# Kernel tuning notes

Hardware: AMD Instinct MI355X
Metric: run time of the kernel (lower is better)

Reference implementation:

```python
import jax, jax.numpy as jnp
import numpy as np

N_NODES = 50000
N_EDGES = 800000
IN_DIM, HID_DIM, N_CLASS = 128, 128, 2
DROPOUT_P = 0.5
NEG_SLOPE = 0.01  # F.leaky_relu default


def gcn_conv(x, src, dst, W, b, n_nodes):
    """PyG GCNConv: add self-loops, sym-normalize, aggregate, then bias."""
    loops = jnp.arange(n_nodes, dtype=src.dtype)
    s = jnp.concatenate([src, loops])
    d = jnp.concatenate([dst, loops])
    # degree on A + I (edge weights = 1), counted at destination
    deg = jax.ops.segment_sum(jnp.ones_like(d, dtype=x.dtype), d, num_segments=n_nodes)
    dis = jnp.where(deg > 0, jax.lax.rsqrt(deg), 0.0)  # deg^{-1/2}
    norm = dis[s] * dis[d]                               # [E+N]
    h = x @ W                                            # [N, out]
    msg = h[s] * norm[:, None]                           # gather + scale
    out = jax.ops.segment_sum(msg, d, num_segments=n_nodes)  # scatter-add
    return out + b


def dropout(x, p, key):
    keep = 1.0 - p
    mask = jax.random.bernoulli(key, keep, x.shape)
    return jnp.where(mask, x / keep, 0.0)


def setup_inputs() -> dict:
    key = jax.random.key(0)
    ks = jax.random.split(key, 8)
    x = jax.random.normal(ks[0], (N_NODES, IN_DIM), dtype=jnp.float32)
    edge_index = jax.random.randint(ks[1], (2, N_EDGES), 0, N_NODES, dtype=jnp.int64)
    def glorot(k, fin, fout):
        lim = np.sqrt(6.0 / (fin + fout)).astype(np.float32)
        return jax.random.uniform(k, (fin, fout), jnp.float32, -lim, lim)
    W1 = glorot(ks[2], IN_DIM, HID_DIM)
    W2 = glorot(ks[3], HID_DIM, HID_DIM)
    W3 = glorot(ks[4], HID_DIM, N_CLASS)
    b1 = jnp.zeros((HID_DIM,), jnp.float32)
    b2 = jnp.zeros((HID_DIM,), jnp.float32)
    b3 = jnp.zeros((N_CLASS,), jnp.float32)
    return {"x": x, "edge_index": edge_index, "W1": W1, "b1": b1,
            "W2": W2, "b2": b2, "W3": W3, "b3": b3}


def reference(x, edge_index, W1, b1, W2, b2, W3, b3):
    src, dst = edge_index[0], edge_index[1]
    n = x.shape[0]
    dkey = jax.random.key(42)
    k1, k2 = jax.random.split(dkey)
    h = gcn_conv(x, src, dst, W1, b1, n)
    h = jax.nn.leaky_relu(h, NEG_SLOPE)
    h = dropout(h, DROPOUT_P, k1)
    h = gcn_conv(h, src, dst, W2, b2, n)
    h = jax.nn.leaky_relu(h, NEG_SLOPE)
    h = dropout(h, DROPOUT_P, k2)
    h = gcn_conv(h, src, dst, W3, b3, n)
    return jax.nn.log_softmax(h, axis=1)
```

## Files before the change

### kernel.cpp

```cpp
#include <hip/hip_runtime.h>
#include <stdint.h>

#define N_NODES 50000
#define N_EDGES 800000
#define DIM     128
#define NB   196
#define CAP  8192
#define CHUNK 2048
#define NBLK 391
#define GNODES 16
#define GGRID 3125
#define GCAP 2048
#define FN   64
#define FBLK 782
#define GCAP_F 3072
#define G3NODES 128
#define G3CAP 4096
#define ZBLK 98

typedef __attribute__((ext_vector_type(8))) unsigned short ushort8_t;
typedef __attribute__((ext_vector_type(8))) short bfrag;
typedef __attribute__((ext_vector_type(4))) float f32x4;

__host__ __device__ inline void threefry2x32(uint32_t k0, uint32_t k1,
                                             uint32_t x0, uint32_t x1,
                                             uint32_t& o0, uint32_t& o1) {
    uint32_t ks0 = k0, ks1 = k1, ks2 = k0 ^ k1 ^ 0x1BD11BDAu;
    uint32_t v0 = x0 + ks0, v1 = x1 + ks1;
#define TF_R(r) { v0 += v1; v1 = (v1 << (r)) | (v1 >> (32 - (r))); v1 ^= v0; }
    TF_R(13) TF_R(15) TF_R(26) TF_R(6)
    v0 += ks1; v1 += ks2 + 1u;
    TF_R(17) TF_R(29) TF_R(16) TF_R(24)
    v0 += ks2; v1 += ks0 + 2u;
    TF_R(13) TF_R(15) TF_R(26) TF_R(6)
    v0 += ks0; v1 += ks1 + 3u;
    TF_R(17) TF_R(29) TF_R(16) TF_R(24)
    v0 += ks1; v1 += ks2 + 4u;
    TF_R(13) TF_R(15) TF_R(26) TF_R(6)
    v0 += ks2; v1 += ks0 + 5u;
#undef TF_R
    o0 = v0; o1 = v1;
}

__device__ inline float drop_scale(uint32_t kk0, uint32_t kk1, uint32_t i) {
    uint32_t b0, b1;
    threefry2x32(kk0, kk1, 0u, i, b0, b1);
    uint32_t bits = b0 ^ b1;
    return (bits >> 31) ? 0.0f : 2.0f;
}

__device__ inline float bf2f(ushort u) {
    return __uint_as_float(((uint32_t)u) << 16);
}
__device__ inline float bfpair_lo(uint32_t u) { return __uint_as_float(u << 16); }
__device__ inline float bfpair_hi(uint32_t u) { return __uint_as_float(u & 0xffff0000u); }

__device__ inline ushort f2bf_rne(float f) {
    uint32_t bits = __float_as_uint(f);
    uint32_t lsb = (bits >> 16) & 1u;
    bits += 0x7fffu + lsb;
    return (ushort)(bits >> 16);
}

__device__ inline void acc8(float* acc, uint4 u, float d) {
    acc[0] += d * bfpair_lo(u.x); acc[1] += d * bfpair_hi(u.x);
    acc[2] += d * bfpair_lo(u.y); acc[3] += d * bfpair_hi(u.y);
    acc[4] += d * bfpair_lo(u.z); acc[5] += d * bfpair_hi(u.z);
    acc[6] += d * bfpair_lo(u.w); acc[7] += d * bfpair_hi(u.w);
}
__device__ inline void acc8p(float* acc, uint4 u) {
    acc[0] += bfpair_lo(u.x); acc[1] += bfpair_hi(u.x);
    acc[2] += bfpair_lo(u.y); acc[3] += bfpair_hi(u.y);
    acc[4] += bfpair_lo(u.z); acc[5] += bfpair_hi(u.z);
    acc[6] += bfpair_lo(u.w); acc[7] += bfpair_hi(u.w);
}

template<int F32A, int SCALE>
__device__ inline void gemm_body(const ushort* __restrict__ Xb,
                                 const float* __restrict__ Xf,
                                 const ushort* __restrict__ Wt,
                                 const float* __restrict__ dis,
                                 ushort* __restrict__ Hb, int gb, int tid) {
    int w = tid >> 6, lane = tid & 63;
    int m0 = gb * 128 + w * 32;
    int lrow = lane & 15, quad = lane >> 4;
    f32x4 acc[2][8] = {};
    for (int kt = 0; kt < DIM; kt += 32) {
        bfrag a[2], b[8];
        #pragma unroll
        for (int t = 0; t < 2; ++t) {
            int m = m0 + t * 16 + lrow;
            if (m >= N_NODES) m = 0;
            if (F32A) {
                const float* p = Xf + (size_t)m * DIM + kt + quad * 8;
                f32x4 v0 = *(const f32x4*)p;
                f32x4 v1 = *(const f32x4*)(p + 4);
                #pragma unroll
                for (int j = 0; j < 4; ++j) {
                    a[t][j]     = (short)f2bf_rne(v0[j]);
                    a[t][j + 4] = (short)f2bf_rne(v1[j]);
                }
            } else {
                a[t] = *(const bfrag*)(Xb + (size_t)m * DIM + kt + quad * 8);
            }
        }
        #pragma unroll
        for (int c = 0; c < 8; ++c) {
            int n = c * 16 + lrow;
            b[c] = *(const bfrag*)(Wt + (size_t)n * DIM + kt + quad * 8);
        }
        #pragma unroll
        for (int t = 0; t < 2; ++t)
            #pragma unroll
            for (int c = 0; c < 8; ++c)
                acc[t][c] = __builtin_amdgcn_mfma_f32_16x16x32_bf16(a[t], b[c], acc[t][c], 0, 0, 0);
    }
    #pragma unroll
    for (int t = 0; t < 2; ++t) {
        #pragma unroll
        for (int r = 0; r < 4; ++r) {
            int rowi = m0 + t * 16 + quad * 4 + r;
            if (rowi < N_NODES) {
                float dv = SCALE ? dis[rowi] : 1.0f;
                #pragma unroll
                for (int c = 0; c < 8; ++c) {
                    int feat = c * 16 + lrow;
                    float z = SCALE ? acc[t][c][r] * dv : acc[t][c][r];
                    Hb[(size_t)rowi * DIM + feat] = f2bf_rne(z);
                }
            }
        }
    }
}

__global__ __launch_bounds__(256) void k_prep(const float* __restrict__ W1,
                                              const float* __restrict__ W2,
                                              ushort* __restrict__ W1t,
                                              ushort* __restrict__ W2t,
                                              const int* __restrict__ src,
                                              const int* __restrict__ dst,
                                              uint32_t* __restrict__ gcur,
                                              uint32_t* __restrict__ packed,
                                              float* __restrict__ h3s) {
    __shared__ uint32_t h[NB];
    int b = blockIdx.x;
    int t = threadIdx.x;
    if (b < NBLK) {
        uint32_t dc[CHUNK / 256], sc[CHUNK / 256];
        if (t < NB) h[t] = 0u;
        __syncthreads();
        int base = b * CHUNK;
        #pragma unroll
        for (int i = 0; i < CHUNK / 256; ++i) {
            int e = base + i * 256 + t;
            if (e < N_EDGES) {
                dc[i] = (uint32_t)dst[e];
                sc[i] = (uint32_t)src[e];
                atomicAdd(&h[dc[i] >> 8], 1u);
            } else {
                dc[i] = 0xffffffffu;
            }
        }
        __syncthreads();
        if (t < NB) {
            uint32_t c = h[t];
            h[t] = c ? atomicAdd(&gcur[t], c) : 0u;
        }
        __syncthreads();
        #pragma unroll
        for (int i = 0; i < CHUNK / 256; ++i) {
            if (dc[i] != 0xffffffffu) {
                uint32_t d = dc[i];
                uint32_t s = sc[i];
                uint32_t bk = d >> 8;
                uint32_t pos = atomicAdd(&h[bk], 1u);
                if (pos < CAP)
                    packed[(size_t)bk * CAP + pos] = ((d & 255u) << 16) | s;
            }
        }
    } else if (b < NBLK + 128) {
        int j = (b - NBLK) * 256 + t;
        const float* W = (j < DIM * DIM) ? W1 : W2;
        ushort* Wt = (j < DIM * DIM) ? W1t : W2t;
        int i = j & (DIM * DIM - 1);
        int k = i >> 7, n = i & 127;
        Wt[n * DIM + k] = f2bf_rne(W[k * DIM + n]);
    } else {
        int idx = (b - NBLK - 128) * 256 + t;
        if (idx < (N_NODES * 2) / 4) {
            f32x4 z = {0.f, 0.f, 0.f, 0.f};
            ((f32x4*)h3s)[idx] = z;
        }
    }
}

__global__ __launch_bounds__(256) void k_fill(const uint32_t* __restrict__ gcur,
                                              const uint32_t* __restrict__ packed,
                                              uint32_t* __restrict__ row,
                                              float* __restrict__ dis,
                                              ushort* __restrict__ col16,
                                              const float* __restrict__ x,
                                              const ushort* __restrict__ W1t,
                                              ushort* __restrict__ Hb) {
    __shared__ uint32_t sdeg[256];
    __shared__ uint32_t scan[256];
    __shared__ uint32_t cur[256];
    int b = blockIdx.x;
    int t = threadIdx.x;
    if (b >= NB) {
        gemm_body<1, 0>(nullptr, x, W1t, nullptr, Hb, b - NB, t);
        return;
    }
    uint32_t n = gcur[b];
    scan[t] = (t < b) ? gcur[t] : 0u;
    __syncthreads();
    for (int off = 1; off < 256; off <<= 1) {
        uint32_t xx = (t >= off) ? scan[t - off] : 0u;
        __syncthreads();
        scan[t] += xx;
        __syncthreads();
    }
    uint32_t cbase = scan[255];
    __syncthreads();
    uint32_t pbase = (uint32_t)b * CAP;
    sdeg[t] = 0u;
    __syncthreads();
    for (uint32_t i = t; i < n; i += 256) {
        uint32_t u = packed[pbase + i];
        atomicAdd(&sdeg[u >> 16], 1u);
    }
    __syncthreads();
    uint32_t myd = sdeg[t];
    scan[t] = myd;
    __syncthreads();
    for (int off = 1; off < 256; off <<= 1) {
        uint32_t xx = (t >= off) ? scan[t - off] : 0u;
        __syncthreads();
        scan[t] += xx;
        __syncthreads();
    }
    uint32_t excl = scan[t] - myd;
    cur[t] = excl;
    int v = b * 256 + t;
    if (v <= N_NODES) row[v] = cbase + excl;
    if (v < N_NODES)  dis[v] = 1.0f / sqrtf((float)(myd + 1u));
    __syncthreads();
    for (uint32_t i = t; i < n; i += 256) {
        uint32_t u = packed[pbase + i];
        uint32_t pos = cbase + atomicAdd(&cur[u >> 16], 1u);
        col16[pos] = (ushort)(u & 0xffffu);
    }
}

__global__ __launch_bounds__(256) void k_fused(const uint32_t* __restrict__ row,
                                               const ushort* __restrict__ col16,
                                               const float* __restrict__ dis,
                                               const ushort* __restrict__ Hb,
                                               const float* __restrict__ bias,
                                               ushort* __restrict__ Bs,
                                               const ushort* __restrict__ W2t,
                                               ushort* __restrict__ Hb2,
                                               uint32_t kk0, uint32_t kk1) {
    __shared__ ushort scol[GCAP_F];
    __shared__ uint32_t srow[FN + 1];
    int tid = threadIdx.x;
    int nbase = blockIdx.x * FN;
    int top = N_NODES - nbase; if (top > FN) top = FN;
    for (int i = tid; i <= top; i += 256) srow[i] = row[nbase + i];
    __syncthreads();
    uint32_t eLo = srow[0];
    uint32_t count = srow[top] - eLo;
    bool staged = count <= GCAP_F;
    if (staged) {
        for (uint32_t i = tid; i < count; i += 256) scol[i] = col16[eLo + i];
    }
    __syncthreads();

    int nl = tid >> 4;
    int q  = tid & 15;
    #pragma unroll
    for (int r = 0; r < 4; ++r) {
        int lr = r * 16 + nl;
        int v = nbase + lr;
        if (lr < top) {
            float dv = dis[v];
            float acc[8];
            {
                uint4 u = *(const uint4*)(Hb + (size_t)v * DIM + q * 8);
                acc[0] = bfpair_lo(u.x); acc[1] = bfpair_hi(u.x);
                acc[2] = bfpair_lo(u.y); acc[3] = bfpair_hi(u.y);
                acc[4] = bfpair_lo(u.z); acc[5] = bfpair_hi(u.z);
                acc[6] = bfpair_lo(u.w); acc[7] = bfpair_hi(u.w);
                #pragma unroll
                for (int j = 0; j < 8; ++j) acc[j] *= dv;
            }
            uint32_t e0 = srow[lr] - eLo, e1 = srow[lr + 1] - eLo;
            uint32_t e = e0;
            if (staged) {
                for (; e + 8 <= e1; e += 8) {
                    uint32_t s0 = scol[e],     s1 = scol[e + 1];
                    uint32_t s2 = scol[e + 2], s3 = scol[e + 3];
                    uint32_t s4 = scol[e + 4], s5 = scol[e + 5];
                    uint32_t s6 = scol[e + 6], s7 = scol[e + 7];
                    uint4 u0 = *(const uint4*)(Hb + (size_t)s0 * DIM + q * 8);
                    uint4 u1 = *(const uint4*)(Hb + (size_t)s1 * DIM + q * 8);
                    uint4 u2 = *(const uint4*)(Hb + (size_t)s2 * DIM + q * 8);
                    uint4 u3 = *(const uint4*)(Hb + (size_t)s3 * DIM + q * 8);
                    uint4 u4 = *(const uint4*)(Hb + (size_t)s4 * DIM + q * 8);
                    uint4 u5 = *(const uint4*)(Hb + (size_t)s5 * DIM + q * 8);
                    uint4 u6 = *(const uint4*)(Hb + (size_t)s6 * DIM + q * 8);
                    uint4 u7 = *(const uint4*)(Hb + (size_t)s7 * DIM + q * 8);
                    float d0 = dis[s0], d1 = dis[s1], d2 = dis[s2], d3 = dis[s3];
                    float d4 = dis[s4], d5 = dis[s5], d6 = dis[s6], d7 = dis[s7];
                    acc8(acc, u0, d0); acc8(acc, u1, d1);
                    acc8(acc, u2, d2); acc8(acc, u3, d3);
                    acc8(acc, u4, d4); acc8(acc, u5, d5);
                    acc8(acc, u6, d6); acc8(acc, u7, d7);
                }
                for (; e + 4 <= e1; e += 4) {
                    uint32_t s0 = scol[e],     s1 = scol[e + 1];
                    uint32_t s2 = scol[e + 2], s3 = scol[e + 3];
                    uint4 u0 = *(const uint4*)(Hb + (size_t)s0 * DIM + q * 8);
                    uint4 u1 = *(const uint4*)(Hb + (size_t)s1 * DIM + q * 8);
                    uint4 u2 = *(const uint4*)(Hb + (size_t)s2 * DIM + q * 8);
                    uint4 u3 = *(const uint4*)(Hb + (size_t)s3 * DIM + q * 8);
                    float d0 = dis[s0], d1 = dis[s1], d2 = dis[s2], d3 = dis[s3];
                    acc8(acc, u0, d0); acc8(acc, u1, d1);
                    acc8(acc, u2, d2); acc8(acc, u3, d3);
                }
                for (; e < e1; ++e) {
                    uint32_t s0 = scol[e];
                    uint4 u0 = *(const uint4*)(Hb + (size_t)s0 * DIM + q * 8);
                    acc8(acc, u0, dis[s0]);
                }
            } else {
                for (; e < e1; ++e) {
                    uint32_t s0 = col16[eLo + e];
                    uint4 u0 = *(const uint4*)(Hb + (size_t)s0 * DIM + q * 8);
                    acc8(acc, u0, dis[s0]);
                }
            }
            int cbase = q * 8;
            uint32_t ibase = (uint32_t)(v * DIM + cbase);
            ushort8_t o;
            #pragma unroll
            for (int j = 0; j < 8; ++j) {
                float z = acc[j] * dv + bias[cbase + j];
                z = (z >= 0.f) ? z : 0.01f * z;
                z *= drop_scale(kk0, kk1, ibase + j);
                o[j] = f2bf_rne(z);
            }
            *((ushort8_t*)(Bs + (size_t)v * DIM + cbase)) = o;
        }
    }
    __syncthreads();

    int w = tid >> 6, lane = tid & 63;
    int lrow = lane & 15, quad = lane >> 4;
    int m = nbase + w * 16 + lrow;
    const ushort* Arow = Bs + (size_t)m * DIM;
    #pragma unroll
    for (int half = 0; half < 2; ++half) {
        f32x4 acc[4] = {};
        for (int kt = 0; kt < DIM; kt += 32) {
            bfrag a = *(const bfrag*)(Arow + kt + quad * 8);
            #pragma unroll
            for (int c = 0; c < 4; ++c) {
                int n = (half * 4 + c) * 16 + lrow;
                bfrag b = *(const bfrag*)(W2t + (size_t)n * DIM + kt + quad * 8);
                acc[c] = __builtin_amdgcn_mfma_f32_16x16x32_bf16(a, b, acc[c], 0, 0, 0);
            }
        }
        #pragma unroll
        for (int rr = 0; rr < 4; ++rr) {
            int rowi = nbase + w * 16 + quad * 4 + rr;
            if (rowi < N_NODES) {
                float dvv = dis[rowi];
                #pragma unroll
                for (int c = 0; c < 4; ++c) {
                    int feat = (half * 4 + c) * 16 + lrow;
                    Hb2[(size_t)rowi * DIM + feat] = f2bf_rne(acc[c][rr] * dvv);
                }
            }
        }
    }
}

__global__ __launch_bounds__(256) void k_gather2(const uint32_t* __restrict__ row,
                                                 const ushort* __restrict__ col16,
                                                 const float* __restrict__ dis,
                                                 const ushort* __restrict__ Hb,
                                                 const float* __restrict__ bias,
                                                 const float* __restrict__ W3,
                                                 float* __restrict__ h3s,
                                                 uint32_t kk0, uint32_t kk1) {
    __shared__ ushort scol[GCAP];
    __shared__ uint32_t srow[GNODES + 1];
    int tid = threadIdx.x;
    int nbase = blockIdx.x * GNODES;
    if (tid <= GNODES) srow[tid] = row[nbase + tid];
    __syncthreads();
    uint32_t eLo = srow[0];
    uint32_t count = srow[GNODES] - eLo;
    bool staged = count <= GCAP;
    if (staged) {
        for (uint32_t i = tid; i < count; i += 256) scol[i] = col16[eLo + i];
    }
    __syncthreads();

    int nl = tid >> 4;
    int q  = tid & 15;
    int v = nbase + nl;
    float dv = dis[v];
    float acc[8];
    {
        uint4 u = *(const uint4*)(Hb + (size_t)v * DIM + q * 8);
        acc[0] = bfpair_lo(u.x); acc[1] = bfpair_hi(u.x);
        acc[2] = bfpair_lo(u.y); acc[3] = bfpair_hi(u.y);
        acc[4] = bfpair_lo(u.z); acc[5] = bfpair_hi(u.z);
        acc[6] = bfpair_lo(u.w); acc[7] = bfpair_hi(u.w);
    }

    uint32_t e0 = srow[nl] - eLo, e1 = srow[nl + 1] - eLo;
    uint32_t e = e0;
    if (staged) {
        for (; e + 8 <= e1; e += 8) {
            uint32_t s0 = scol[e],     s1 = scol[e + 1];
            uint32_t s2 = scol[e + 2], s3 = scol[e + 3];
            uint32_t s4 = scol[e + 4], s5 = scol[e + 5];
            uint32_t s6 = scol[e + 6], s7 = scol[e + 7];
            uint4 u0 = *(const uint4*)(Hb + (size_t)s0 * DIM + q * 8);
            uint4 u1 = *(const uint4*)(Hb + (size_t)s1 * DIM + q * 8);
            uint4 u2 = *(const uint4*)(Hb + (size_t)s2 * DIM + q * 8);
            uint4 u3 = *(const uint4*)(Hb + (size_t)s3 * DIM + q * 8);
            uint4 u4 = *(const uint4*)(Hb + (size_t)s4 * DIM + q * 8);
            uint4 u5 = *(const uint4*)(Hb + (size_t)s5 * DIM + q * 8);
            uint4 u6 = *(const uint4*)(Hb + (size_t)s6 * DIM + q * 8);
            uint4 u7 = *(const uint4*)(Hb + (size_t)s7 * DIM + q * 8);
            acc8p(acc, u0); acc8p(acc, u1); acc8p(acc, u2); acc8p(acc, u3);
            acc8p(acc, u4); acc8p(acc, u5); acc8p(acc, u6); acc8p(acc, u7);
        }
        for (; e + 4 <= e1; e += 4) {
            uint32_t s0 = scol[e],     s1 = scol[e + 1];
            uint32_t s2 = scol[e + 2], s3 = scol[e + 3];
            uint4 u0 = *(const uint4*)(Hb + (size_t)s0 * DIM + q * 8);
            uint4 u1 = *(const uint4*)(Hb + (size_t)s1 * DIM + q * 8);
            uint4 u2 = *(const uint4*)(Hb + (size_t)s2 * DIM + q * 8);
            uint4 u3 = *(const uint4*)(Hb + (size_t)s3 * DIM + q * 8);
            acc8p(acc, u0); acc8p(acc, u1); acc8p(acc, u2); acc8p(acc, u3);
        }
        for (; e < e1; ++e) {
            uint4 u0 = *(const uint4*)(Hb + (size_t)scol[e] * DIM + q * 8);
            acc8p(acc, u0);
        }
    } else {
        for (; e < e1; ++e) {
            uint4 u0 = *(const uint4*)(Hb + (size_t)col16[eLo + e] * DIM + q * 8);
            acc8p(acc, u0);
        }
    }

    int cbase = q * 8;
    uint32_t ibase = (uint32_t)(v * DIM + cbase);
    float o0 = 0.f, o1 = 0.f;
    #pragma unroll
    for (int j = 0; j < 8; ++j) {
        float z = acc[j] * dv + bias[cbase + j];
        z = (z >= 0.f) ? z : 0.01f * z;
        z *= drop_scale(kk0, kk1, ibase + j);
        o0 += z * W3[(cbase + j) * 2 + 0];
        o1 += z * W3[(cbase + j) * 2 + 1];
    }
    o0 += __shfl_xor(o0, 1); o0 += __shfl_xor(o0, 2);
    o0 += __shfl_xor(o0, 4); o0 += __shfl_xor(o0, 8);
    o1 += __shfl_xor(o1, 1); o1 += __shfl_xor(o1, 2);
    o1 += __shfl_xor(o1, 4); o1 += __shfl_xor(o1, 8);
    if (q == 0) {
        atomicAdd(&h3s[v * 2 + 0], o0 * dv);
        atomicAdd(&h3s[v * 2 + 1], o1 * dv);
    }
}

__global__ __launch_bounds__(256) void k_gather3(const uint32_t* __restrict__ row,
                                                 const ushort* __restrict__ col16,
                                                 const float* __restrict__ dis,
                                                 const float* __restrict__ H3s,
                                                 const float* __restrict__ b3,
                                                 float* __restrict__ out) {
    __shared__ ushort scol[G3CAP];
    __shared__ uint32_t srow[G3NODES + 1];
    int tid = threadIdx.x;
    int nbase = blockIdx.x * G3NODES;
    int nend = nbase + G3NODES; if (nend > N_NODES) nend = N_NODES;
    int nloc = nend - nbase;
    for (int i = tid; i <= nloc; i += 256) srow[i] = row[nbase + i];
    __syncthreads();
    uint32_t eLo = srow[0];
    uint32_t count = srow[nloc] - eLo;
    bool staged = count <= G3CAP;
    if (staged) {
        for (uint32_t i = tid; i < count; i += 256) scol[i] = col16[eLo + i];
    }
    __syncthreads();

    int nl = tid >> 1;
    int par = tid & 1;
    int v = nbase + nl;
    if (v >= N_NODES) return;
    const float2* H2 = (const float2*)H3s;
    float z0 = 0.f, z1 = 0.f;
    if (par == 0) {
        float2 h = H2[v];
        z0 = h.x; z1 = h.y;
    }
    uint32_t e0 = srow[nl] - eLo, e1 = srow[nl + 1] - eLo;
    if (staged) {
        for (uint32_t e = e0 + par; e < e1; e += 2) {
            float2 ha = H2[scol[e]];
            z0 += ha.x; z1 += ha.y;
        }
    } else {
        for (uint32_t e = e0 + par; e < e1; e += 2) {
            float2 ha = H2[col16[eLo + e]];
            z0 += ha.x; z1 += ha.y;
        }
    }
    z0 += __shfl_xor(z0, 1);
    z1 += __shfl_xor(z1, 1);
    if (par) return;
    float dv = dis[v];
    z0 = z0 * dv + b3[0];
    z1 = z1 * dv + b3[1];
    float m = fmaxf(z0, z1);
    float lse = m + logf(expf(z0 - m) + expf(z1 - m));
    out[v * 2 + 0] = z0 - lse;
    out[v * 2 + 1] = z1 - lse;
}

extern "C" void kernel_launch(void* const* d_in, const int* in_sizes, int n_in,
                              void* d_out, int out_size, void* d_ws, size_t ws_size,
                              hipStream_t stream) {
    const float* x  = (const float*)d_in[0];
    const int*   ei = (const int*)d_in[1];
    const float* W1 = (const float*)d_in[2];
    const float* b1 = (const float*)d_in[3];
    const float* W2 = (const float*)d_in[4];
    const float* b2 = (const float*)d_in[5];
    const float* W3 = (const float*)d_in[6];
    const float* b3 = (const float*)d_in[7];
    float* out = (float*)d_out;

    const int* src = ei;
    const int* dst = ei + N_EDGES;

    uint32_t* wsu = (uint32_t*)d_ws;
    float*    wsf = (float*)d_ws;
    uint32_t* gcur   = wsu;
    uint32_t* row    = wsu + 256;
    float*    dis    = wsf + 50304;
    uint32_t* packed = wsu + 100352;
    ushort*   col16  = (ushort*)(wsu + 1705984);
    ushort*   Hb     = (ushort*)(wsu + 2106112);
    ushort*   Bs     = (ushort*)(wsu + 5306112);
    ushort*   Hb2    = (ushort*)(wsu + 8506112);
    ushort*   W1t    = (ushort*)(wsu + 11706112);
    ushort*   W2t    = (ushort*)(wsu + 11714304);
    float*    h3s    = wsf + 11722496;

    uint32_t k1a, k1b, k2a, k2b;
    threefry2x32(0u, 42u, 0u, 0u, k1a, k1b);
    threefry2x32(0u, 42u, 0u, 1u, k2a, k2b);

    hipMemsetAsync(gcur, 0, 256 * sizeof(uint32_t), stream);

    k_prep<<<NBLK + 128 + ZBLK, 256, 0, stream>>>(W1, W2, W1t, W2t,
                                                  src, dst, gcur, packed, h3s);

    k_fill<<<NB + 391, 256, 0, stream>>>(gcur, packed, row, dis, col16,
                                         x, W1t, Hb);

    k_fused<<<FBLK, 256, 0, stream>>>(row, col16, dis, Hb, b1, Bs, W2t, Hb2,
                                      k1a, k1b);

    k_gather2<<<GGRID, 256, 0, stream>>>(row, col16, dis, Hb2, b2, W3, h3s,
                                         k2a, k2b);

    k_gather3<<<(N_NODES + G3NODES - 1) / G3NODES, 256, 0, stream>>>(row, col16, dis,
                                                                     h3s, b3, out);
}
```

Before: 212.7 us.

## Keep layer-1 activations in swizzled LDS and shrink fused block to 16 nodes

The fused layer-1 aggregation plus layer-2 GEMM kernel now processes 16 nodes per block instead of 64. The activated, dropped-out bf16 rows go into an XOR-swizzled shared-memory tile rather than a global scratch buffer (Bs). Each of the four waves then computes two 16-column output tiles of the MFMA GEMM, reading A from LDS. This removes a global write and read-back of a 50000x128 bf16 array and raises the block count for better latency hiding, at the cost of less W2 reuse per block and more per-block overhead.

```diff
diff --git a/kernel.cpp b/kernel.cpp
--- a/kernel.cpp
+++ b/kernel.cpp
@@ -11,9 +11,6 @@
 #define GNODES 16
 #define GGRID 3125
 #define GCAP 2048
-#define FN   64
-#define FBLK 782
-#define GCAP_F 3072
 #define G3NODES 128
 #define G3CAP 4096
 #define ZBLK 98
@@ -257,20 +254,19 @@
                                                const float* __restrict__ dis,
                                                const ushort* __restrict__ Hb,
                                                const float* __restrict__ bias,
-                                               ushort* __restrict__ Bs,
                                                const ushort* __restrict__ W2t,
                                                ushort* __restrict__ Hb2,
                                                uint32_t kk0, uint32_t kk1) {
-    __shared__ ushort scol[GCAP_F];
-    __shared__ uint32_t srow[FN + 1];
+    __shared__ ushort scol[GCAP];
+    __shared__ uint32_t srow[GNODES + 1];
+    __shared__ ushort At[GNODES * DIM];
     int tid = threadIdx.x;
-    int nbase = blockIdx.x * FN;
-    int top = N_NODES - nbase; if (top > FN) top = FN;
-    for (int i = tid; i <= top; i += 256) srow[i] = row[nbase + i];
+    int nbase = blockIdx.x * GNODES;
+    if (tid <= GNODES) srow[tid] = row[nbase + tid];
     __syncthreads();
     uint32_t eLo = srow[0];
-    uint32_t count = srow[top] - eLo;
-    bool staged = count <= GCAP_F;
+    uint32_t count = srow[GNODES] - eLo;
+    bool staged = count <= GCAP;
     if (staged) {
         for (uint32_t i = tid; i < count; i += 256) scol[i] = col16[eLo + i];
     }
@@ -278,110 +274,101 @@
 
     int nl = tid >> 4;
     int q  = tid & 15;
-    #pragma unroll
-    for (int r = 0; r < 4; ++r) {
-        int lr = r * 16 + nl;
-        int v = nbase + lr;
-        if (lr < top) {
-            float dv = dis[v];
-            float acc[8];
-            {
-                uint4 u = *(const uint4*)(Hb + (size_t)v * DIM + q * 8);
-                acc[0] = bfpair_lo(u.x); acc[1] = bfpair_hi(u.x);
-                acc[2] = bfpair_lo(u.y); acc[3] = bfpair_hi(u.y);
-                acc[4] = bfpair_lo(u.z); acc[5] = bfpair_hi(u.z);
-                acc[6] = bfpair_lo(u.w); acc[7] = bfpair_hi(u.w);
-                #pragma unroll
-                for (int j = 0; j < 8; ++j) acc[j] *= dv;
-            }
-            uint32_t e0 = srow[lr] - eLo, e1 = srow[lr + 1] - eLo;
-            uint32_t e = e0;
-            if (staged) {
-                for (; e + 8 <= e1; e += 8) {
-                    uint32_t s0 = scol[e],     s1 = scol[e + 1];
-                    uint32_t s2 = scol[e + 2], s3 = scol[e + 3];
-                    uint32_t s4 = scol[e + 4], s5 = scol[e + 5];
-                    uint32_t s6 = scol[e + 6], s7 = scol[e + 7];
-                    uint4 u0 = *(const uint4*)(Hb + (size_t)s0 * DIM + q * 8);
-                    uint4 u1 = *(const uint4*)(Hb + (size_t)s1 * DIM + q * 8);
-                    uint4 u2 = *(const uint4*)(Hb + (size_t)s2 * DIM + q * 8);
-                    uint4 u3 = *(const uint4*)(Hb + (size_t)s3 * DIM + q * 8);
-                    uint4 u4 = *(const uint4*)(Hb + (size_t)s4 * DIM + q * 8);
-                    uint4 u5 = *(const uint4*)(Hb + (size_t)s5 * DIM + q * 8);
-                    uint4 u6 = *(const uint4*)(Hb + (size_t)s6 * DIM + q * 8);
-                    uint4 u7 = *(const uint4*)(Hb + (size_t)s7 * DIM + q * 8);
-                    float d0 = dis[s0], d1 = dis[s1], d2 = dis[s2], d3 = dis[s3];
-                    float d4 = dis[s4], d5 = dis[s5], d6 = dis[s6], d7 = dis[s7];
-                    acc8(acc, u0, d0); acc8(acc, u1, d1);
-                    acc8(acc, u2, d2); acc8(acc, u3, d3);
-                    acc8(acc, u4, d4); acc8(acc, u5, d5);
-                    acc8(acc, u6, d6); acc8(acc, u7, d7);
-                }
-                for (; e + 4 <= e1; e += 4) {
-                    uint32_t s0 = scol[e],     s1 = scol[e + 1];
-                    uint32_t s2 = scol[e + 2], s3 = scol[e + 3];
-                    uint4 u0 = *(const uint4*)(Hb + (size_t)s0 * DIM + q * 8);
-                    uint4 u1 = *(const uint4*)(Hb + (size_t)s1 * DIM + q * 8);
-                    uint4 u2 = *(const uint4*)(Hb + (size_t)s2 * DIM + q * 8);
-                    uint4 u3 = *(const uint4*)(Hb + (size_t)s3 * DIM + q * 8);
-                    float d0 = dis[s0], d1 = dis[s1], d2 = dis[s2], d3 = dis[s3];
-                    acc8(acc, u0, d0); acc8(acc, u1, d1);
-                    acc8(acc, u2, d2); acc8(acc, u3, d3);
-                }
-                for (; e < e1; ++e) {
-                    uint32_t s0 = scol[e];
-                    uint4 u0 = *(const uint4*)(Hb + (size_t)s0 * DIM + q * 8);
-                    acc8(acc, u0, dis[s0]);
-                }
-            } else {
-                for (; e < e1; ++e) {
-                    uint32_t s0 = col16[eLo + e];
-                    uint4 u0 = *(const uint4*)(Hb + (size_t)s0 * DIM + q * 8);
-                    acc8(acc, u0, dis[s0]);
-                }
-            }
-            int cbase = q * 8;
-            uint32_t ibase = (uint32_t)(v * DIM + cbase);
-            ushort8_t o;
-            #pragma unroll
-            for (int j = 0; j < 8; ++j) {
-                float z = acc[j] * dv + bias[cbase + j];
-                z = (z >= 0.f) ? z : 0.01f * z;
-                z *= drop_scale(kk0, kk1, ibase + j);
-                o[j] = f2bf_rne(z);
-            }
-            *((ushort8_t*)(Bs + (size_t)v * DIM + cbase)) = o;
-        }
+    int v = nbase + nl;
+    float dv = dis[v];
+    float acc[8];
+    {
+        uint4 u = *(const uint4*)(Hb + (size_t)v * DIM + q * 8);
+        acc[0] = bfpair_lo(u.x); acc[1] = bfpair_hi(u.x);
+        acc[2] = bfpair_lo(u.y); acc[3] = bfpair_hi(u.y);
+        acc[4] = bfpair_lo(u.z); acc[5] = bfpair_hi(u.z);
+        acc[6] = bfpair_lo(u.w); acc[7] = bfpair_hi(u.w);
+        #pragma unroll
+        for (int j = 0; j < 8; ++j) acc[j] *= dv;
+    }
+    uint32_t e0 = srow[nl] - eLo, e1 = srow[nl + 1] - eLo;
+    uint32_t e = e0;
+    if (staged) {
+        for (; e + 8 <= e1; e += 8) {
+            uint32_t s0 = scol[e],     s1 = scol[e + 1];
+            uint32_t s2 = scol[e + 2], s3 = scol[e + 3];
+            uint32_t s4 = scol[e + 4], s5 = scol[e + 5];
+            uint32_t s6 = scol[e + 6], s7 = scol[e + 7];
+            uint4 u0 = *(const uint4*)(Hb + (size_t)s0 * DIM + q * 8);
+            uint4 u1 = *(const uint4*)(Hb + (size_t)s1 * DIM + q * 8);
+            uint4 u2 = *(const uint4*)(Hb + (size_t)s2 * DIM + q * 8);
+            uint4 u3 = *(const uint4*)(Hb + (size_t)s3 * DIM + q * 8);
+            uint4 u4 = *(const uint4*)(Hb + (size_t)s4 * DIM + q * 8);
+            uint4 u5 = *(const uint4*)(Hb + (size_t)s5 * DIM + q * 8);
+            uint4 u6 = *(const uint4*)(Hb + (size_t)s6 * DIM + q * 8);
+            uint4 u7 = *(const uint4*)(Hb + (size_t)s7 * DIM + q * 8);
+            float d0 = dis[s0], d1 = dis[s1], d2 = dis[s2], d3 = dis[s3];
+            float d4 = dis[s4], d5 = dis[s5], d6 = dis[s6], d7 = dis[s7];
+            acc8(acc, u0, d0); acc8(acc, u1, d1);
+            acc8(acc, u2, d2); acc8(acc, u3, d3);
+            acc8(acc, u4, d4); acc8(acc, u5, d5);
+            acc8(acc, u6, d6); acc8(acc, u7, d7);
+        }
+        for (; e + 4 <= e1; e += 4) {
+            uint32_t s0 = scol[e],     s1 = scol[e + 1];
+            uint32_t s2 = scol[e + 2], s3 = scol[e + 3];
+            uint4 u0 = *(const uint4*)(Hb + (size_t)s0 * DIM + q * 8);
+            uint4 u1 = *(const uint4*)(Hb + (size_t)s1 * DIM + q * 8);
+            uint4 u2 = *(const uint4*)(Hb + (size_t)s2 * DIM + q * 8);
+            uint4 u3 = *(const uint4*)(Hb + (size_t)s3 * DIM + q * 8);
+            float d0 = dis[s0], d1 = dis[s1], d2 = dis[s2], d3 = dis[s3];
+            acc8(acc, u0, d0); acc8(acc, u1, d1);
+            acc8(acc, u2, d2); acc8(acc, u3, d3);
+        }
+        for (; e < e1; ++e) {
+            uint32_t s0 = scol[e];
+            uint4 u0 = *(const uint4*)(Hb + (size_t)s0 * DIM + q * 8);
+            acc8(acc, u0, dis[s0]);
+        }
+    } else {
+        for (; e < e1; ++e) {
+            uint32_t s0 = col16[eLo + e];
+            uint4 u0 = *(const uint4*)(Hb + (size_t)s0 * DIM + q * 8);
+            acc8(acc, u0, dis[s0]);
+        }
+    }
+    {
+        int cbase = q * 8;
+        uint32_t ibase = (uint32_t)(v * DIM + cbase);
+        ushort8_t o;
+        #pragma unroll
+        for (int j = 0; j < 8; ++j) {
+            float z = acc[j] * dv + bias[cbase + j];
+            z = (z >= 0.f) ? z : 0.01f * z;
+            z *= drop_scale(kk0, kk1, ibase + j);
+            o[j] = f2bf_rne(z);
+        }
+        *((ushort8_t*)(At + nl * DIM + ((q * 8) ^ ((nl & 7) << 3)))) = o;
     }
     __syncthreads();
 
     int w = tid >> 6, lane = tid & 63;
     int lrow = lane & 15, quad = lane >> 4;
-    int m = nbase + w * 16 + lrow;
-    const ushort* Arow = Bs + (size_t)m * DIM;
+    int swz = (lrow & 7) << 3;
+    f32x4 acc2[2] = {};
+    for (int kt = 0; kt < DIM; kt += 32) {
+        int k = kt + quad * 8;
+        bfrag a = *(const bfrag*)(At + lrow * DIM + (k ^ swz));
+        #pragma unroll
+        for (int ct = 0; ct < 2; ++ct) {
+            int n = (w * 2 + ct) * 16 + lrow;
+            bfrag b = *(const bfrag*)(W2t + (size_t)n * DIM + k);
+            acc2[ct] = __builtin_amdgcn_mfma_f32_16x16x32_bf16(a, b, acc2[ct], 0, 0, 0);
+        }
+    }
     #pragma unroll
-    for (int half = 0; half < 2; ++half) {
-        f32x4 acc[4] = {};
-        for (int kt = 0; kt < DIM; kt += 32) {
-            bfrag a = *(const bfrag*)(Arow + kt + quad * 8);
-            #pragma unroll
-            for (int c = 0; c < 4; ++c) {
-                int n = (half * 4 + c) * 16 + lrow;
-                bfrag b = *(const bfrag*)(W2t + (size_t)n * DIM + kt + quad * 8);
-                acc[c] = __builtin_amdgcn_mfma_f32_16x16x32_bf16(a, b, acc[c], 0, 0, 0);
-            }
-        }
+    for (int ct = 0; ct < 2; ++ct) {
         #pragma unroll
         for (int rr = 0; rr < 4; ++rr) {
-            int rowi = nbase + w * 16 + quad * 4 + rr;
-            if (rowi < N_NODES) {
-                float dvv = dis[rowi];
-                #pragma unroll
-                for (int c = 0; c < 4; ++c) {
-                    int feat = (half * 4 + c) * 16 + lrow;
-                    Hb2[(size_t)rowi * DIM + feat] = f2bf_rne(acc[c][rr] * dvv);
-                }
-            }
+            int rowi = nbase + quad * 4 + rr;
+            float dvv = dis[rowi];
+            int feat = (w * 2 + ct) * 16 + lrow;
+            Hb2[(size_t)rowi * DIM + feat] = f2bf_rne(acc2[ct][rr] * dvv);
         }
     }
 }
@@ -561,7 +548,6 @@
     uint32_t* packed = wsu + 100352;
     ushort*   col16  = (ushort*)(wsu + 1705984);
     ushort*   Hb     = (ushort*)(wsu + 2106112);
-    ushort*   Bs     = (ushort*)(wsu + 5306112);
     ushort*   Hb2    = (ushort*)(wsu + 8506112);
     ushort*   W1t    = (ushort*)(wsu + 11706112);
     ushort*   W2t    = (ushort*)(wsu + 11714304);
@@ -579,8 +565,8 @@
     k_fill<<<NB + 391, 256, 0, stream>>>(gcur, packed, row, dis, col16,
                                          x, W1t, Hb);
 
-    k_fused<<<FBLK, 256, 0, stream>>>(row, col16, dis, Hb, b1, Bs, W2t, Hb2,
-                                      k1a, k1b);
+    k_fused<<<GGRID, 256, 0, stream>>>(row, col16, dis, Hb, b1, W2t, Hb2,
+                                       k1a, k1b);
 
     k_gather2<<<GGRID, 256, 0, stream>>>(row, col16, dis, Hb2, b2, W3, h3s,
                                          k2a, k2b);
```

Result: faster. 204.2 us (-4.0%).
